# Kernel optimization log

Measured on AMD Instinct MI355X. Metric: run time of the kernel, lower is better.

The kernel has to match this reference:

```python
import jax, jax.numpy as jnp
import numpy as np

B, T, D, H, OUT = 256, 512, 512, 1024, 8


def setup_inputs() -> dict:
    key = jax.random.key(0)
    ks = jax.random.split(key, 7)
    s_ih = 1.0 / np.sqrt(H)
    return {
        "x": jax.random.normal(ks[0], (B, T, D), dtype=jnp.float32),
        "W_ih": jax.random.uniform(ks[1], (4 * H, D), minval=-s_ih, maxval=s_ih, dtype=jnp.float32),
        "W_hh": jax.random.uniform(ks[2], (4 * H, H), minval=-s_ih, maxval=s_ih, dtype=jnp.float32),
        "b_ih": jax.random.uniform(ks[3], (4 * H,), minval=-s_ih, maxval=s_ih, dtype=jnp.float32),
        "b_hh": jax.random.uniform(ks[4], (4 * H,), minval=-s_ih, maxval=s_ih, dtype=jnp.float32),
        "W_fc": jax.random.uniform(ks[5], (OUT, H), minval=-s_ih, maxval=s_ih, dtype=jnp.float32),
        "b_fc": jax.random.uniform(ks[6], (OUT,), minval=-s_ih, maxval=s_ih, dtype=jnp.float32),
    }


def reference(x, W_ih, W_hh, b_ih, b_hh, W_fc, b_fc):
    Bsz, Tlen, _ = x.shape
    Hd = W_hh.shape[1]
    # Precompute input-side gate projections for all time steps: [T, B, 4H]
    x_proj = jnp.einsum('btd,gd->tbg', x, W_ih) + b_ih + b_hh

    def step(carry, xp):
        h, c = carry
        gates = xp + h @ W_hh.T                 # [B, 4H]
        i, f, g, o = jnp.split(gates, 4, axis=-1)  # torch LSTMCell gate order
        i = jax.nn.sigmoid(i)
        f = jax.nn.sigmoid(f)
        g = jnp.tanh(g)
        o = jax.nn.sigmoid(o)
        c = f * c + i * g
        h = o * jnp.tanh(c)
        return (h, c), None

    h0 = jnp.zeros((Bsz, Hd), dtype=x.dtype)
    c0 = jnp.zeros((Bsz, Hd), dtype=x.dtype)
    (h, _), _ = jax.lax.scan(step, (h0, c0), x_proj)
    out = h @ W_fc.T + b_fc
    return jax.nn.sigmoid(out)
```

## Files before the change

kernel.cpp:

```cpp
#include <hip/hip_runtime.h>
#include <hip/hip_bf16.h>

#define Bsz 256
#define Tlen 512
#define Dd 512
#define Hh 1024
#define G4 4096
#define NOUT 8
#define BT (Bsz * Tlen)

typedef short s16x8 __attribute__((ext_vector_type(8)));
typedef unsigned short u16x8 __attribute__((ext_vector_type(8)));
typedef float f32x4 __attribute__((ext_vector_type(4)));

__device__ __forceinline__ ushort f2bf(float f) {
    union { float f; uint u; } v; v.f = f;
    uint u = v.u;
    uint r = u + 0x7FFFu + ((u >> 16) & 1u);
    return (ushort)(r >> 16);
}
__device__ __forceinline__ float bf2f(ushort u) {
    union { uint u; float f; } v; v.u = ((uint)u) << 16; return v.f;
}
__device__ __forceinline__ float sigf(float x) { return 1.f / (1.f + __expf(-x)); }
__device__ __forceinline__ float tanhfast(float x) {
    float ax = fabsf(x);
    float e = __expf(-2.f * ax);
    float t = (1.f - e) / (1.f + e);
    return copysignf(t, x);
}
__device__ __forceinline__ void gload16(const void* g, void* l) {
    __builtin_amdgcn_global_load_lds(
        (const __attribute__((address_space(1))) uint*)g,
        (__attribute__((address_space(3))) uint*)l, 16, 0, 0);
}

__global__ void init_kernel(uint4* __restrict__ h0, uint4* __restrict__ c) {
    int i = blockIdx.x * 256 + threadIdx.x;
    uint4 z = make_uint4(0u, 0u, 0u, 0u);
    c[i] = z;
    if (i < 32768) h0[i] = z;
}

__global__ void cvt_kernel(const float4* __restrict__ src, ushort4* __restrict__ dst, int n4) {
    int i = blockIdx.x * 256 + threadIdx.x;
    if (i >= n4) return;
    float4 v = src[i];
    ushort4 o;
    o.x = f2bf(v.x); o.y = f2bf(v.y); o.z = f2bf(v.z); o.w = f2bf(v.w);
    dst[i] = o;
}

__global__ void cvt_xchunk(const float* __restrict__ x, ushort* __restrict__ dst, int t0) {
    int gid = blockIdx.x * 256 + threadIdx.x;
    int k8  = gid & 63;
    int tl  = (gid >> 6) & 7;
    int row = gid >> 9;
    const float* s = x + ((size_t)row * Tlen + t0 + tl) * Dd + k8 * 8;
    float4 v0 = *(const float4*)s;
    float4 v1 = *(const float4*)(s + 4);
    u16x8 o;
    o[0]=f2bf(v0.x); o[1]=f2bf(v0.y); o[2]=f2bf(v0.z); o[3]=f2bf(v0.w);
    o[4]=f2bf(v1.x); o[5]=f2bf(v1.y); o[6]=f2bf(v1.z); o[7]=f2bf(v1.w);
    *(u16x8*)(dst + ((size_t)row * 8 + tl) * Dd + k8 * 8) = o;
}

__launch_bounds__(512, 2)
__global__ void lstm_step3(const ushort* __restrict__ xsrc, int tstride, int tloc,
                           const ushort* __restrict__ Wih,
                           const ushort* __restrict__ Whh,
                           const ushort* __restrict__ h_prev,
                           ushort* __restrict__ h_next,
                           float* __restrict__ c,
                           const float* __restrict__ b_ih,
                           const float* __restrict__ b_hh) {
    __shared__ char smem[131072];
    __shared__ float bias_lds[64];

    const int tid  = threadIdx.x;
    const int lane = tid & 63;
    const int w    = tid >> 6;
    const int g    = w >> 1;
    const int ab   = w & 1;

    const int B   = blockIdx.x;
    const int xcd  = B & 7, slot = B >> 3;
    const int jt   = xcd * 8 + (slot >> 2);
    const int bt   = slot & 3;
    const int b0   = bt * 64;

    if (tid < 64) {
        int gcol = (tid >> 4) * 1024 + jt * 16 + (tid & 15);
        bias_lds[tid] = b_ih[gcol] + b_hh[gcol];
    }

    f32x4 acc[4][2] = {};

    auto STAGE = [&](int buf, int it) {
        const int k0 = (g * 6 + it) << 6;
        char* base = smem + g * 32768 + buf * 16384 + ab * 8192;
        if (ab == 0) {
            if (k0 < Dd) {
                #pragma unroll
                for (int q = 0; q < 8; ++q) {
                    int r  = q * 8 + (lane >> 3);
                    int cs = (lane & 7) ^ (r & 7);
                    const ushort* gp = xsrc + ((size_t)(b0 + r) * tstride + tloc) * Dd + k0 + cs * 8;
                    gload16(gp, base + q * 1024);
                }
            } else {
                #pragma unroll
                for (int q = 0; q < 8; ++q) {
                    int r  = q * 8 + (lane >> 3);
                    int cs = (lane & 7) ^ (r & 7);
                    const ushort* gp = h_prev + (size_t)(b0 + r) * Hh + (k0 - Dd) + cs * 8;
                    gload16(gp, base + q * 1024);
                }
            }
        } else {
            #pragma unroll
            for (int q = 0; q < 8; ++q) {
                int col = q * 8 + (lane >> 3);
                int cs  = (lane & 7) ^ (col & 7);
                int grow = (col >> 4) * 1024 + jt * 16 + (col & 15);
                const ushort* gp = (k0 < Dd)
                    ? (Wih + (size_t)grow * Dd + k0 + cs * 8)
                    : (Whh + (size_t)grow * Hh + (k0 - Dd) + cs * 8);
                gload16(gp, base + q * 1024);
            }
        }
    };
    auto COMPUTE = [&](int buf) {
        const char* Ab = smem + g * 32768 + buf * 16384;
        const char* Bb = Ab + 8192;
        #pragma unroll
        for (int ks = 0; ks < 2; ++ks) {
            const int kc = (ks << 2) + (lane >> 4);
            s16x8 a[4], bb[2];
            #pragma unroll
            for (int m = 0; m < 4; ++m) {
                int row = (m << 4) + (lane & 15);
                a[m] = *(const s16x8*)(Ab + row * 128 + ((kc ^ (row & 7)) << 4));
            }
            #pragma unroll
            for (int n = 0; n < 2; ++n) {
                int col = (ab << 5) + (n << 4) + (lane & 15);
                bb[n] = *(const s16x8*)(Bb + col * 128 + ((kc ^ (col & 7)) << 4));
            }
            #pragma unroll
            for (int m = 0; m < 4; ++m)
                #pragma unroll
                for (int n = 0; n < 2; ++n)
                    acc[m][n] = __builtin_amdgcn_mfma_f32_16x16x32_bf16(a[m], bb[n], acc[m][n], 0, 0, 0);
        }
    };

    STAGE(0, 0);
    __syncthreads();
    #pragma unroll
    for (int it = 0; it < 6; ++it) {
        if (it < 5) STAGE((it + 1) & 1, it + 1);
        COMPUTE(it & 1);
        __syncthreads();
    }

    float* bw = (float*)smem + g * (64 * 68);
    #pragma unroll
    for (int m = 0; m < 4; ++m)
        #pragma unroll
        for (int n = 0; n < 2; ++n)
            #pragma unroll
            for (int j = 0; j < 4; ++j) {
                int row = (m << 4) + ((lane >> 4) << 2) + j;
                int col = (ab << 5) + (n << 4) + (lane & 15);
                bw[row * 68 + col] = acc[m][n][j];
            }
    __syncthreads();

    const float* bufs = (const float*)smem;
    #pragma unroll
    for (int u = 0; u < 2; ++u) {
        int cell = tid * 2 + u;
        int row  = cell >> 4;
        int cv   = cell & 15;
        float gi = 0.f, gf = 0.f, gg = 0.f, go = 0.f;
        #pragma unroll
        for (int p = 0; p < 4; ++p) {
            const float* bb = bufs + p * (64 * 68) + row * 68;
            gi += bb[cv]; gf += bb[16 + cv]; gg += bb[32 + cv]; go += bb[48 + cv];
        }
        gi += bias_lds[cv];      gf += bias_lds[16 + cv];
        gg += bias_lds[32 + cv]; go += bias_lds[48 + cv];
        float i_ = sigf(gi), f_ = sigf(gf), g_ = tanhfast(gg), o_ = sigf(go);
        int gcol = jt * 16 + cv;
        size_t cidx = (size_t)(b0 + row) * Hh + gcol;
        float cn = f_ * c[cidx] + i_ * g_;
        c[cidx] = cn;
        h_next[cidx] = f2bf(o_ * tanhfast(cn));
    }
}

__launch_bounds__(256)
__global__ void lstm_step_fused(const float* __restrict__ x,
                          const ushort* __restrict__ Wih,
                          const ushort* __restrict__ Whh,
                          const float* __restrict__ b_ih,
                          const float* __restrict__ b_hh,
                          const ushort* __restrict__ h_prev,
                          ushort* __restrict__ h_next,
                          float* __restrict__ c,
                          int t) {
    __shared__ ushort At[64 * 64];
    __shared__ ushort Bt[64 * 64];
    __shared__ float gates[64 * 72];

    const int tid  = threadIdx.x;
    const int lane = tid & 63;
    const int wid  = tid >> 6;
    const int wr   = wid >> 1;
    const int wc   = wid & 1;
    const int bt   = blockIdx.x >> 6;
    const int jt   = blockIdx.x & 63;
    const int b0   = bt * 64;
    const int j0   = jt * 16;

    f32x4 acc[2][2] = {};

    auto mfma_tile = [&]() {
        #pragma unroll
        for (int ks = 0; ks < 2; ++ks) {
            const int kc = (ks << 2) + (lane >> 4);
            s16x8 a[2], bfr[2];
            #pragma unroll
            for (int m = 0; m < 2; ++m) {
                int row = wr * 32 + m * 16 + (lane & 15);
                a[m] = *(const s16x8*)&At[row * 64 + ((kc ^ (row & 7)) << 3)];
            }
            #pragma unroll
            for (int n = 0; n < 2; ++n) {
                int col = wc * 32 + n * 16 + (lane & 15);
                bfr[n] = *(const s16x8*)&Bt[col * 64 + ((kc ^ (col & 7)) << 3)];
            }
            #pragma unroll
            for (int m = 0; m < 2; ++m)
                #pragma unroll
                for (int n = 0; n < 2; ++n)
                    acc[m][n] = __builtin_amdgcn_mfma_f32_16x16x32_bf16(a[m], bfr[n], acc[m][n], 0, 0, 0);
        }
    };

    for (int kb = 0; kb < Dd; kb += 64) {
        __syncthreads();
        #pragma unroll
        for (int it = 0; it < 4; ++it) {
            int idx = tid + it * 256;
            int row = idx >> 4;
            int k   = (idx & 15) * 4;
            const float4 v = *(const float4*)&x[(size_t)(b0 + row) * (Tlen * Dd) + (size_t)t * Dd + kb + k];
            ushort4 o;
            o.x = f2bf(v.x); o.y = f2bf(v.y); o.z = f2bf(v.z); o.w = f2bf(v.w);
            int dst = row * 64 + (((k >> 3) ^ (row & 7)) << 3) + (k & 7);
            *(ushort4*)&At[dst] = o;
        }
        #pragma unroll
        for (int it = 0; it < 2; ++it) {
            int idx = tid + it * 256;
            int col = idx >> 3;
            int kc  = idx & 7;
            int grow = ((col >> 4) << 10) + j0 + (col & 15);
            uint4 v = *(const uint4*)&Wih[(size_t)grow * Dd + kb + kc * 8];
            *(uint4*)&Bt[col * 64 + ((kc ^ (col & 7)) << 3)] = v;
        }
        __syncthreads();
        mfma_tile();
    }
    for (int kb = 0; kb < Hh; kb += 64) {
        __syncthreads();
        #pragma unroll
        for (int it = 0; it < 2; ++it) {
            int idx = tid + it * 256;
            int row = idx >> 3;
            int kc  = idx & 7;
            uint4 v = *(const uint4*)&h_prev[(size_t)(b0 + row) * Hh + kb + kc * 8];
            *(uint4*)&At[row * 64 + ((kc ^ (row & 7)) << 3)] = v;
        }
        #pragma unroll
        for (int it = 0; it < 2; ++it) {
            int idx = tid + it * 256;
            int col = idx >> 3;
            int kc  = idx & 7;
            int grow = ((col >> 4) << 10) + j0 + (col & 15);
            uint4 v = *(const uint4*)&Whh[(size_t)grow * Hh + kb + kc * 8];
            *(uint4*)&Bt[col * 64 + ((kc ^ (col & 7)) << 3)] = v;
        }
        __syncthreads();
        mfma_tile();
    }

    #pragma unroll
    for (int m = 0; m < 2; ++m)
        #pragma unroll
        for (int n = 0; n < 2; ++n)
            #pragma unroll
            for (int j = 0; j < 4; ++j) {
                int row = wr * 32 + m * 16 + ((lane >> 4) << 2) + j;
                int col = wc * 32 + n * 16 + (lane & 15);
                gates[row * 72 + col] = acc[m][n][j];
            }
    __syncthreads();

    #pragma unroll
    for (int it = 0; it < 4; ++it) {
        int idx = tid + it * 256;
        int row = idx >> 4;
        int cc  = idx & 15;
        int gcol = j0 + cc;
        float gi = gates[row * 72 + cc]      + b_ih[gcol]          + b_hh[gcol];
        float gf = gates[row * 72 + 16 + cc] + b_ih[Hh + gcol]     + b_hh[Hh + gcol];
        float gg = gates[row * 72 + 32 + cc] + b_ih[2 * Hh + gcol] + b_hh[2 * Hh + gcol];
        float go = gates[row * 72 + 48 + cc] + b_ih[3 * Hh + gcol] + b_hh[3 * Hh + gcol];
        float i_ = sigf(gi);
        float f_ = sigf(gf);
        float g_ = tanhfast(gg);
        float o_ = sigf(go);
        size_t cidx = (size_t)(b0 + row) * Hh + gcol;
        float cn = f_ * c[cidx] + i_ * g_;
        c[cidx] = cn;
        float hn = o_ * tanhfast(cn);
        h_next[cidx] = f2bf(hn);
    }
}

__global__ void fc_kernel(const ushort* __restrict__ h,
                          const float* __restrict__ Wfc,
                          const float* __restrict__ bfc,
                          float* __restrict__ out) {
    int b = blockIdx.x;
    int w = threadIdx.x >> 6;
    int lane = threadIdx.x & 63;
    float s = 0.f;
    for (int k = lane; k < Hh; k += 64)
        s += bf2f(h[(size_t)b * Hh + k]) * Wfc[w * Hh + k];
    #pragma unroll
    for (int off = 32; off; off >>= 1) s += __shfl_down(s, off);
    if (lane == 0) out[b * NOUT + w] = sigf(s + bfc[w]);
}


extern "C" void kernel_launch(void* const* d_in, const int* in_sizes, int n_in,
                              void* d_out, int out_size, void* d_ws, size_t ws_size,
                              hipStream_t stream) {
    const float* x    = (const float*)d_in[0];
    const float* W_ih = (const float*)d_in[1];
    const float* W_hh = (const float*)d_in[2];
    const float* b_ih = (const float*)d_in[3];
    const float* b_hh = (const float*)d_in[4];
    const float* W_fc = (const float*)d_in[5];
    const float* b_fc = (const float*)d_in[6];
    float* out = (float*)d_out;
    char* ws = (char*)d_ws;

    ushort* h_buf  = (ushort*)ws;
    float*  c_ws   = (float*)(ws + (1ull << 20));
    ushort* wih_bf = (ushort*)(ws + (2ull << 20));
    ushort* whh_bf = (ushort*)(ws + (6ull << 20));
    char*   x_ext  = ws + (14ull << 20);

    const size_t FIXED   = 14ull << 20;
    const size_t XFULL   = (size_t)Bsz * Tlen * Dd * 2;
    const size_t XCHUNK  = (size_t)Bsz * 8 * Dd * 2;

    init_kernel<<<256, 256, 0, stream>>>((uint4*)h_buf, (uint4*)c_ws);
    cvt_kernel<<<(G4 * Dd / 4) / 256, 256, 0, stream>>>((const float4*)W_ih, (ushort4*)wih_bf, G4 * Dd / 4);
    cvt_kernel<<<(G4 * Hh / 4) / 256, 256, 0, stream>>>((const float4*)W_hh, (ushort4*)whh_bf, G4 * Hh / 4);

    if (ws_size >= FIXED + XFULL) {
        ushort* x_bf = (ushort*)x_ext;
        const int n4 = BT * Dd / 4;
        cvt_kernel<<<n4 / 256, 256, 0, stream>>>((const float4*)x, (ushort4*)x_bf, n4);
        for (int t = 0; t < Tlen; ++t) {
            const ushort* hp = h_buf + (size_t)(t & 1) * Bsz * Hh;
            ushort*       hn = h_buf + (size_t)((t + 1) & 1) * Bsz * Hh;
            lstm_step3<<<256, 512, 0, stream>>>(x_bf, Tlen, t, wih_bf, whh_bf,
                                                hp, hn, c_ws, b_ih, b_hh);
        }
    } else if (ws_size >= FIXED + 2 * XCHUNK) {
        ushort* xchunk = (ushort*)x_ext;
        for (int t = 0; t < Tlen; ++t) {
            if ((t & 7) == 0) {
                ushort* dst = xchunk + (size_t)((t >> 3) & 1) * (Bsz * 8 * Dd);
                cvt_xchunk<<<512, 256, 0, stream>>>(x, dst, t);
            }
            const ushort* xb = xchunk + (size_t)((t >> 3) & 1) * (Bsz * 8 * Dd);
            const ushort* hp = h_buf + (size_t)(t & 1) * Bsz * Hh;
            ushort*       hn = h_buf + (size_t)((t + 1) & 1) * Bsz * Hh;
            lstm_step3<<<256, 512, 0, stream>>>(xb, 8, t & 7, wih_bf, whh_bf,
                                                hp, hn, c_ws, b_ih, b_hh);
        }
    } else {
        for (int t = 0; t < Tlen; ++t) {
            const ushort* hp = h_buf + (size_t)(t & 1) * Bsz * Hh;
            ushort*       hn = h_buf + (size_t)((t + 1) & 1) * Bsz * Hh;
            lstm_step_fused<<<256, 256, 0, stream>>>(x, wih_bf, whh_bf, b_ih, b_hh, hp, hn, c_ws, t);
        }
    }
    fc_kernel<<<256, 512, 0, stream>>>(h_buf, W_fc, b_fc, out);
}
```

Baseline: 5.618 ms.

## Load LSTM step operands directly into registers and split K across all eight waves

The per-step kernel no longer stages x/h and weight tiles through LDS with global_load_lds double buffering. Each of the 8 waves now owns 3 of the 24 K-chunks and loads A and B fragments straight from global memory into registers, with a two-deep software prefetch ahead of the MFMAs. Each wave computes the full 64x64 output tile, and the partial sums are reduced across 8 LDS buffers instead of 4. The aim is to drop LDS staging traffic and barriers inside the K loop. In exchange it uses more registers, issues uncoalesced 16-byte global loads without LDS reuse, and doubles the reduction work.

```diff
diff --git a/kernel.cpp b/kernel.cpp
--- a/kernel.cpp
+++ b/kernel.cpp
@@ -28,11 +28,6 @@
     float e = __expf(-2.f * ax);
     float t = (1.f - e) / (1.f + e);
     return copysignf(t, x);
-}
-__device__ __forceinline__ void gload16(const void* g, void* l) {
-    __builtin_amdgcn_global_load_lds(
-        (const __attribute__((address_space(1))) uint*)g,
-        (__attribute__((address_space(3))) uint*)l, 16, 0, 0);
 }
 
 __global__ void init_kernel(uint4* __restrict__ h0, uint4* __restrict__ c) {
@@ -66,7 +61,7 @@
 }
 
 __launch_bounds__(512, 2)
-__global__ void lstm_step3(const ushort* __restrict__ xsrc, int tstride, int tloc,
+__global__ void lstm_step4(const ushort* __restrict__ xsrc, int tstride, int tloc,
                            const ushort* __restrict__ Wih,
                            const ushort* __restrict__ Whh,
                            const ushort* __restrict__ h_prev,
@@ -74,16 +69,13 @@
                            float* __restrict__ c,
                            const float* __restrict__ b_ih,
                            const float* __restrict__ b_hh) {
-    __shared__ char smem[131072];
+    __shared__ float part[8][64 * 68];
     __shared__ float bias_lds[64];
 
     const int tid  = threadIdx.x;
     const int lane = tid & 63;
     const int w    = tid >> 6;
-    const int g    = w >> 1;
-    const int ab   = w & 1;
-
-    const int B   = blockIdx.x;
+    const int B    = blockIdx.x;
     const int xcd  = B & 7, slot = B >> 3;
     const int jt   = xcd * 8 + (slot >> 2);
     const int bt   = slot & 3;
@@ -94,106 +86,88 @@
         bias_lds[tid] = b_ih[gcol] + b_hh[gcol];
     }
 
-    f32x4 acc[4][2] = {};
-
-    auto STAGE = [&](int buf, int it) {
-        const int k0 = (g * 6 + it) << 6;
-        char* base = smem + g * 32768 + buf * 16384 + ab * 8192;
-        if (ab == 0) {
-            if (k0 < Dd) {
-                #pragma unroll
-                for (int q = 0; q < 8; ++q) {
-                    int r  = q * 8 + (lane >> 3);
-                    int cs = (lane & 7) ^ (r & 7);
-                    const ushort* gp = xsrc + ((size_t)(b0 + r) * tstride + tloc) * Dd + k0 + cs * 8;
-                    gload16(gp, base + q * 1024);
-                }
-            } else {
-                #pragma unroll
-                for (int q = 0; q < 8; ++q) {
-                    int r  = q * 8 + (lane >> 3);
-                    int cs = (lane & 7) ^ (r & 7);
-                    const ushort* gp = h_prev + (size_t)(b0 + r) * Hh + (k0 - Dd) + cs * 8;
-                    gload16(gp, base + q * 1024);
-                }
-            }
-        } else {
-            #pragma unroll
-            for (int q = 0; q < 8; ++q) {
-                int col = q * 8 + (lane >> 3);
-                int cs  = (lane & 7) ^ (col & 7);
-                int grow = (col >> 4) * 1024 + jt * 16 + (col & 15);
-                const ushort* gp = (k0 < Dd)
-                    ? (Wih + (size_t)grow * Dd + k0 + cs * 8)
-                    : (Whh + (size_t)grow * Hh + (k0 - Dd) + cs * 8);
-                gload16(gp, base + q * 1024);
+    const int rlo = lane & 15;
+    const int k8  = (lane >> 4) << 3;
+
+    auto loadA = [&](s16x8 (&a)[4][2], int cidx) {
+        const int kc = cidx << 6;
+        #pragma unroll
+        for (int ks = 0; ks < 2; ++ks) {
+            const int k = kc + (ks << 5) + k8;
+            #pragma unroll
+            for (int m = 0; m < 4; ++m) {
+                const int row = b0 + (m << 4) + rlo;
+                const ushort* p = (k < Dd)
+                    ? xsrc + ((size_t)row * tstride + tloc) * Dd + k
+                    : h_prev + (size_t)row * Hh + (k - Dd);
+                a[m][ks] = *(const s16x8*)p;
             }
         }
     };
-    auto COMPUTE = [&](int buf) {
-        const char* Ab = smem + g * 32768 + buf * 16384;
-        const char* Bb = Ab + 8192;
+    auto loadB = [&](s16x8 (&b)[4][2], int cidx) {
+        const int kc = cidx << 6;
         #pragma unroll
         for (int ks = 0; ks < 2; ++ks) {
-            const int kc = (ks << 2) + (lane >> 4);
-            s16x8 a[4], bb[2];
-            #pragma unroll
-            for (int m = 0; m < 4; ++m) {
-                int row = (m << 4) + (lane & 15);
-                a[m] = *(const s16x8*)(Ab + row * 128 + ((kc ^ (row & 7)) << 4));
-            }
-            #pragma unroll
-            for (int n = 0; n < 2; ++n) {
-                int col = (ab << 5) + (n << 4) + (lane & 15);
-                bb[n] = *(const s16x8*)(Bb + col * 128 + ((kc ^ (col & 7)) << 4));
-            }
+            const int k = kc + (ks << 5) + k8;
+            #pragma unroll
+            for (int n = 0; n < 4; ++n) {
+                const int grow = (n << 10) + (jt << 4) + rlo;
+                const ushort* p = (k < Dd)
+                    ? Wih + (size_t)grow * Dd + k
+                    : Whh + (size_t)grow * Hh + (k - Dd);
+                b[n][ks] = *(const s16x8*)p;
+            }
+        }
+    };
+
+    f32x4 acc[4][4] = {};
+    auto MFMA = [&](s16x8 (&a)[4][2], s16x8 (&b)[4][2]) {
+        #pragma unroll
+        for (int ks = 0; ks < 2; ++ks)
             #pragma unroll
             for (int m = 0; m < 4; ++m)
                 #pragma unroll
-                for (int n = 0; n < 2; ++n)
-                    acc[m][n] = __builtin_amdgcn_mfma_f32_16x16x32_bf16(a[m], bb[n], acc[m][n], 0, 0, 0);
-        }
+                for (int n = 0; n < 4; ++n)
+                    acc[m][n] = __builtin_amdgcn_mfma_f32_16x16x32_bf16(a[m][ks], b[n][ks], acc[m][n], 0, 0, 0);
     };
 
-    STAGE(0, 0);
-    __syncthreads();
-    #pragma unroll
-    for (int it = 0; it < 6; ++it) {
-        if (it < 5) STAGE((it + 1) & 1, it + 1);
-        COMPUTE(it & 1);
-        __syncthreads();
-    }
-
-    float* bw = (float*)smem + g * (64 * 68);
+    const int ch0 = w * 3;
+    s16x8 aA[4][2], bA[4][2], aB[4][2], bB[4][2];
+    loadA(aA, ch0);     loadB(bA, ch0);
+    loadA(aB, ch0 + 1); loadB(bB, ch0 + 1);
+    MFMA(aA, bA);
+    loadA(aA, ch0 + 2); loadB(bA, ch0 + 2);
+    MFMA(aB, bB);
+    MFMA(aA, bA);
+
+    float* bw = part[w];
     #pragma unroll
     for (int m = 0; m < 4; ++m)
         #pragma unroll
-        for (int n = 0; n < 2; ++n)
+        for (int n = 0; n < 4; ++n)
             #pragma unroll
             for (int j = 0; j < 4; ++j) {
                 int row = (m << 4) + ((lane >> 4) << 2) + j;
-                int col = (ab << 5) + (n << 4) + (lane & 15);
+                int col = (n << 4) + rlo;
                 bw[row * 68 + col] = acc[m][n][j];
             }
     __syncthreads();
 
-    const float* bufs = (const float*)smem;
+    const int cv = tid & 15;
+    const int r0 = (tid >> 4) << 1;
     #pragma unroll
     for (int u = 0; u < 2; ++u) {
-        int cell = tid * 2 + u;
-        int row  = cell >> 4;
-        int cv   = cell & 15;
-        float gi = 0.f, gf = 0.f, gg = 0.f, go = 0.f;
-        #pragma unroll
-        for (int p = 0; p < 4; ++p) {
-            const float* bb = bufs + p * (64 * 68) + row * 68;
+        const int row = r0 + u;
+        float gi = bias_lds[cv],      gf = bias_lds[16 + cv];
+        float gg = bias_lds[32 + cv], go = bias_lds[48 + cv];
+        #pragma unroll
+        for (int p = 0; p < 8; ++p) {
+            const float* bb = part[p] + row * 68;
             gi += bb[cv]; gf += bb[16 + cv]; gg += bb[32 + cv]; go += bb[48 + cv];
         }
-        gi += bias_lds[cv];      gf += bias_lds[16 + cv];
-        gg += bias_lds[32 + cv]; go += bias_lds[48 + cv];
         float i_ = sigf(gi), f_ = sigf(gf), g_ = tanhfast(gg), o_ = sigf(go);
-        int gcol = jt * 16 + cv;
-        size_t cidx = (size_t)(b0 + row) * Hh + gcol;
+        const int gcol = (jt << 4) + cv;
+        const size_t cidx = (size_t)(b0 + row) * Hh + gcol;
         float cn = f_ * c[cidx] + i_ * g_;
         c[cidx] = cn;
         h_next[cidx] = f2bf(o_ * tanhfast(cn));
@@ -381,7 +355,7 @@
         for (int t = 0; t < Tlen; ++t) {
             const ushort* hp = h_buf + (size_t)(t & 1) * Bsz * Hh;
             ushort*       hn = h_buf + (size_t)((t + 1) & 1) * Bsz * Hh;
-            lstm_step3<<<256, 512, 0, stream>>>(x_bf, Tlen, t, wih_bf, whh_bf,
+            lstm_step4<<<256, 512, 0, stream>>>(x_bf, Tlen, t, wih_bf, whh_bf,
                                                 hp, hn, c_ws, b_ih, b_hh);
         }
     } else if (ws_size >= FIXED + 2 * XCHUNK) {
@@ -394,7 +368,7 @@
             const ushort* xb = xchunk + (size_t)((t >> 3) & 1) * (Bsz * 8 * Dd);
             const ushort* hp = h_buf + (size_t)(t & 1) * Bsz * Hh;
             ushort*       hn = h_buf + (size_t)((t + 1) & 1) * Bsz * Hh;
-            lstm_step3<<<256, 512, 0, stream>>>(xb, 8, t & 7, wih_bf, whh_bf,
+            lstm_step4<<<256, 512, 0, stream>>>(xb, 8, t & 7, wih_bf, whh_bf,
                                                 hp, hn, c_ws, b_ih, b_hh);
         }
     } else {
```

After: 7.812 ms. 39.0% more time.

## Replace per-timestep launches with a persistent cooperative LSTM kernel using flag barriers

Applied to the files above, without the earlier changes.

Replaces 512 per-timestep kernel launches with one cooperative persistent kernel. Each block keeps its cell state in LDS, converts x to bf16 on the fly, and synchronises with dependent blocks through per-block flags in global memory using sc0/sc1 coherent loads and stores. This is meant to remove launch overhead and the separate x conversion pass. In exchange it relies on all 256 blocks being co-resident and on correct flag ordering, and the spin-wait can add its own latency.

```diff
diff --git a/kernel.cpp b/kernel.cpp
--- a/kernel.cpp
+++ b/kernel.cpp
@@ -12,6 +12,7 @@
 typedef short s16x8 __attribute__((ext_vector_type(8)));
 typedef unsigned short u16x8 __attribute__((ext_vector_type(8)));
 typedef float f32x4 __attribute__((ext_vector_type(4)));
+typedef uint u32x4 __attribute__((ext_vector_type(4)));
 
 __device__ __forceinline__ ushort f2bf(float f) {
     union { float f; uint u; } v; v.f = f;
@@ -33,6 +34,26 @@
     __builtin_amdgcn_global_load_lds(
         (const __attribute__((address_space(1))) uint*)g,
         (__attribute__((address_space(3))) uint*)l, 16, 0, 0);
+}
+__device__ __forceinline__ u32x4 scload16(const void* p) {
+    u32x4 r;
+    asm volatile("global_load_dwordx4 %0, %1, off sc0 sc1" : "=&v"(r) : "v"(p));
+    return r;
+}
+__device__ __forceinline__ int scload_u32(const int* p) {
+    int r;
+    asm volatile("global_load_dword %0, %1, off sc0 sc1\n\ts_waitcnt vmcnt(0)"
+                 : "=&v"(r) : "v"(p) : "memory");
+    return r;
+}
+__device__ __forceinline__ void scstore_u32(uint* p, uint v) {
+    asm volatile("global_store_dword %0, %1, off sc0 sc1" :: "v"(p), "v"(v) : "memory");
+}
+__device__ __forceinline__ u16x8 pack8(const float4& a, const float4& b) {
+    u16x8 o;
+    o[0]=f2bf(a.x); o[1]=f2bf(a.y); o[2]=f2bf(a.z); o[3]=f2bf(a.w);
+    o[4]=f2bf(b.x); o[5]=f2bf(b.y); o[6]=f2bf(b.z); o[7]=f2bf(b.w);
+    return o;
 }
 
 __global__ void init_kernel(uint4* __restrict__ h0, uint4* __restrict__ c) {
@@ -59,10 +80,197 @@
     const float* s = x + ((size_t)row * Tlen + t0 + tl) * Dd + k8 * 8;
     float4 v0 = *(const float4*)s;
     float4 v1 = *(const float4*)(s + 4);
-    u16x8 o;
-    o[0]=f2bf(v0.x); o[1]=f2bf(v0.y); o[2]=f2bf(v0.z); o[3]=f2bf(v0.w);
-    o[4]=f2bf(v1.x); o[5]=f2bf(v1.y); o[6]=f2bf(v1.z); o[7]=f2bf(v1.w);
-    *(u16x8*)(dst + ((size_t)row * 8 + tl) * Dd + k8 * 8) = o;
+    *(u16x8*)(dst + ((size_t)row * 8 + tl) * Dd + k8 * 8) = pack8(v0, v1);
+}
+
+__launch_bounds__(512, 1)
+__global__ void lstm_persist(const float* __restrict__ x,
+                             const ushort* __restrict__ Wih,
+                             const ushort* __restrict__ Whh,
+                             const float* __restrict__ b_ih,
+                             const float* __restrict__ b_hh,
+                             ushort* __restrict__ hbuf,
+                             int* __restrict__ flags) {
+    __shared__ char smem[131072];
+    __shared__ float c_lds[1024];
+    __shared__ float bias_lds[64];
+
+    const int tid  = threadIdx.x;
+    const int lane = tid & 63;
+    const int w    = tid >> 6;
+    const int g    = w >> 1;
+    const int ab   = w & 1;
+    const int B    = blockIdx.x;
+    const int xcd  = B & 7, slot = B >> 3;
+    const int jt   = xcd * 8 + (slot >> 2);
+    const int bt   = slot & 3;
+    const int b0   = bt * 64;
+    const int bidl = (lane >> 3) + ((lane & 7) << 5) + (bt << 3);
+
+    for (int i = tid; i < 1024; i += 512) c_lds[i] = 0.f;
+    if (tid < 64) {
+        int gcol = (tid >> 4) * 1024 + jt * 16 + (tid & 15);
+        bias_lds[tid] = b_ih[gcol] + b_hh[gcol];
+    }
+    __syncthreads();
+
+    char* Abase0 = smem + g * 32768;
+    float4 xv[16];
+    u32x4  hv[8];
+
+    #pragma unroll 1
+    for (int t = 1; t <= Tlen; ++t) {
+        const ushort* hrd = hbuf + (size_t)((t - 1) & 1) * (Bsz * Hh);
+        ushort*       hwr = hbuf + (size_t)(t & 1) * (Bsz * Hh);
+
+        f32x4 acc[4][2] = {};
+
+        auto ISSUE = [&](int it) {
+            const int k0 = g * 384 + it * 64;
+            if (ab == 0) {
+                if (k0 < Dd) {
+                    #pragma unroll
+                    for (int q = 0; q < 8; ++q) {
+                        int row = q * 8 + (lane >> 3);
+                        int cs  = (lane & 7) ^ (row & 7);
+                        const float* p = x + ((size_t)(b0 + row) * Tlen + (t - 1)) * Dd + k0 + cs * 8;
+                        xv[2*q]   = *(const float4*)p;
+                        xv[2*q+1] = *(const float4*)(p + 4);
+                    }
+                } else {
+                    #pragma unroll
+                    for (int q = 0; q < 8; ++q) {
+                        int row = q * 8 + (lane >> 3);
+                        int cs  = (lane & 7) ^ (row & 7);
+                        const ushort* p = hrd + (size_t)(b0 + row) * Hh + (k0 - Dd) + cs * 8;
+                        hv[q] = scload16(p);
+                    }
+                }
+            } else {
+                char* Bb = Abase0 + (it & 1) * 16384 + 8192;
+                #pragma unroll
+                for (int q = 0; q < 8; ++q) {
+                    int col = q * 8 + (lane >> 3);
+                    int cs  = (lane & 7) ^ (col & 7);
+                    int grow = ((col >> 4) << 10) + (jt << 4) + (col & 15);
+                    const ushort* p = (k0 < Dd)
+                        ? Wih + (size_t)grow * Dd + k0 + cs * 8
+                        : Whh + (size_t)grow * Hh + (k0 - Dd) + cs * 8;
+                    gload16(p, Bb + q * 1024);
+                }
+            }
+        };
+        auto WRITE = [&](int it) {
+            if (ab != 0) return;
+            const int k0 = g * 384 + it * 64;
+            char* Ab = Abase0 + (it & 1) * 16384;
+            if (k0 < Dd) {
+                #pragma unroll
+                for (int q = 0; q < 8; ++q)
+                    *(u16x8*)(Ab + q * 1024 + lane * 16) = pack8(xv[2*q], xv[2*q+1]);
+            } else {
+                asm volatile("s_waitcnt vmcnt(0)" ::: "memory");
+                __builtin_amdgcn_sched_barrier(0);
+                #pragma unroll
+                for (int q = 0; q < 8; ++q)
+                    *(u32x4*)(Ab + q * 1024 + lane * 16) = hv[q];
+            }
+        };
+        auto COMPUTE = [&](int buf) {
+            const char* Ab = Abase0 + buf * 16384;
+            const char* Bb = Ab + 8192;
+            #pragma unroll
+            for (int ks = 0; ks < 2; ++ks) {
+                const int kc = (ks << 2) + (lane >> 4);
+                s16x8 a[4], bb2[2];
+                #pragma unroll
+                for (int m = 0; m < 4; ++m) {
+                    int row = (m << 4) + (lane & 15);
+                    a[m] = *(const s16x8*)(Ab + row * 128 + ((kc ^ (row & 7)) << 4));
+                }
+                #pragma unroll
+                for (int n = 0; n < 2; ++n) {
+                    int col = (ab << 5) + (n << 4) + (lane & 15);
+                    bb2[n] = *(const s16x8*)(Bb + col * 128 + ((kc ^ (col & 7)) << 4));
+                }
+                #pragma unroll
+                for (int m = 0; m < 4; ++m)
+                    #pragma unroll
+                    for (int n = 0; n < 2; ++n)
+                        acc[m][n] = __builtin_amdgcn_mfma_f32_16x16x32_bf16(a[m], bb2[n], acc[m][n], 0, 0, 0);
+            }
+        };
+
+        ISSUE(0);
+        WRITE(0);
+        __syncthreads();
+        #pragma unroll
+        for (int it = 0; it < 6; ++it) {
+            if (it < 5) ISSUE(it + 1);
+            COMPUTE(it & 1);
+            if (it < 5) WRITE(it + 1);
+            __syncthreads();
+        }
+
+        float* bw = (float*)smem + g * (64 * 68);
+        #pragma unroll
+        for (int m = 0; m < 4; ++m)
+            #pragma unroll
+            for (int n = 0; n < 2; ++n)
+                #pragma unroll
+                for (int j = 0; j < 4; ++j) {
+                    int row = (m << 4) + ((lane >> 4) << 2) + j;
+                    int col = (ab << 5) + (n << 4) + (lane & 15);
+                    bw[row * 68 + col] = acc[m][n][j];
+                }
+        __syncthreads();
+
+        {
+            const float* part = (const float*)smem;
+            const int cell0 = tid * 2;
+            const int row = cell0 >> 4;
+            const int cv  = cell0 & 15;
+            float gv[2][4];
+            #pragma unroll
+            for (int u = 0; u < 2; ++u) {
+                gv[u][0] = bias_lds[cv + u];
+                gv[u][1] = bias_lds[16 + cv + u];
+                gv[u][2] = bias_lds[32 + cv + u];
+                gv[u][3] = bias_lds[48 + cv + u];
+            }
+            #pragma unroll
+            for (int p = 0; p < 4; ++p) {
+                const float* bb = part + p * (64 * 68) + row * 68;
+                #pragma unroll
+                for (int u = 0; u < 2; ++u) {
+                    gv[u][0] += bb[cv + u];
+                    gv[u][1] += bb[16 + cv + u];
+                    gv[u][2] += bb[32 + cv + u];
+                    gv[u][3] += bb[48 + cv + u];
+                }
+            }
+            ushort hn[2];
+            #pragma unroll
+            for (int u = 0; u < 2; ++u) {
+                float i_ = sigf(gv[u][0]), f_ = sigf(gv[u][1]);
+                float g_ = tanhfast(gv[u][2]), o_ = sigf(gv[u][3]);
+                float cn = f_ * c_lds[row * 16 + cv + u] + i_ * g_;
+                c_lds[row * 16 + cv + u] = cn;
+                hn[u] = f2bf(o_ * tanhfast(cn));
+            }
+            uint pack = (uint)hn[0] | ((uint)hn[1] << 16);
+            scstore_u32((uint*)(hwr + (size_t)(b0 + row) * Hh + (jt << 4) + cv), pack);
+        }
+
+        asm volatile("s_waitcnt vmcnt(0)" ::: "memory");
+        __syncthreads();
+        if (tid == 0) scstore_u32((uint*)&flags[B], (uint)t);
+        for (;;) {
+            int v = scload_u32(&flags[bidl]);
+            if (__all(v >= t)) break;
+            __builtin_amdgcn_s_sleep(4);
+        }
+    }
 }
 
 __launch_bounds__(512, 2)
@@ -362,17 +570,29 @@
 
     ushort* h_buf  = (ushort*)ws;
     float*  c_ws   = (float*)(ws + (1ull << 20));
+    int*    flags  = (int*)(ws + (1ull << 20));
     ushort* wih_bf = (ushort*)(ws + (2ull << 20));
     ushort* whh_bf = (ushort*)(ws + (6ull << 20));
     char*   x_ext  = ws + (14ull << 20);
 
-    const size_t FIXED   = 14ull << 20;
-    const size_t XFULL   = (size_t)Bsz * Tlen * Dd * 2;
-    const size_t XCHUNK  = (size_t)Bsz * 8 * Dd * 2;
+    const size_t FIXED  = 14ull << 20;
+    const size_t XFULL  = (size_t)Bsz * Tlen * Dd * 2;
+    const size_t XCHUNK = (size_t)Bsz * 8 * Dd * 2;
 
     init_kernel<<<256, 256, 0, stream>>>((uint4*)h_buf, (uint4*)c_ws);
     cvt_kernel<<<(G4 * Dd / 4) / 256, 256, 0, stream>>>((const float4*)W_ih, (ushort4*)wih_bf, G4 * Dd / 4);
     cvt_kernel<<<(G4 * Hh / 4) / 256, 256, 0, stream>>>((const float4*)W_hh, (ushort4*)whh_bf, G4 * Hh / 4);
+
+    {
+        void* args[] = { (void*)&x, (void*)&wih_bf, (void*)&whh_bf, (void*)&b_ih,
+                         (void*)&b_hh, (void*)&h_buf, (void*)&flags };
+        hipError_t err = hipLaunchCooperativeKernel((const void*)lstm_persist,
+                                                    dim3(256), dim3(512), args, 0, stream);
+        if (err == hipSuccess) {
+            fc_kernel<<<256, 512, 0, stream>>>(h_buf, W_fc, b_fc, out);
+            return;
+        }
+    }
 
     if (ws_size >= FIXED + XFULL) {
         ushort* x_bf = (ushort*)x_ext;
```

Result: slower. 11.29 ms (+100.9%).

## Hoist input projection into chunked GEMM, shrink per-step kernel to recurrent matmul

Applied to the files above, without the earlier changes.

Moves the x·W_ih projection out of the per-timestep LSTM kernel into a batched MFMA GEMM run every 8 timesteps, which writes gate pre-activations (with both biases) to a double-buffered workspace in fp32 or bf16. The per-step kernel then only multiplies h by W_hh over K=1024 and adds the precomputed projections. This cuts the per-step K dimension and the latency on the serial critical path. In exchange it adds extra launches and more memory traffic to write and read the projection buffers.

```diff
diff --git a/kernel.cpp b/kernel.cpp
--- a/kernel.cpp
+++ b/kernel.cpp
@@ -34,6 +34,10 @@
         (const __attribute__((address_space(1))) uint*)g,
         (__attribute__((address_space(3))) uint*)l, 16, 0, 0);
 }
+__device__ __forceinline__ void xp_store(ushort* p, float v) { *p = f2bf(v); }
+__device__ __forceinline__ void xp_store(float* p, float v) { *p = v; }
+__device__ __forceinline__ float xp_load(const ushort* p) { return bf2f(*p); }
+__device__ __forceinline__ float xp_load(const float* p) { return *p; }
 
 __global__ void init_kernel(uint4* __restrict__ h0, uint4* __restrict__ c) {
     int i = blockIdx.x * 256 + threadIdx.x;
@@ -63,6 +67,222 @@
     o[0]=f2bf(v0.x); o[1]=f2bf(v0.y); o[2]=f2bf(v0.z); o[3]=f2bf(v0.w);
     o[4]=f2bf(v1.x); o[5]=f2bf(v1.y); o[6]=f2bf(v1.z); o[7]=f2bf(v1.w);
     *(u16x8*)(dst + ((size_t)row * 8 + tl) * Dd + k8 * 8) = o;
+}
+
+template <typename XT>
+__launch_bounds__(256)
+__global__ void xproj_chunk(const float* __restrict__ x,
+                            const ushort* __restrict__ Wih,
+                            const float* __restrict__ b_ih,
+                            const float* __restrict__ b_hh,
+                            XT* __restrict__ xp, int t0) {
+    __shared__ ushort As[2][128 * 64];
+    __shared__ ushort Bs[2][128 * 64];
+    const int tid  = threadIdx.x;
+    const int lane = tid & 63;
+    const int wid  = tid >> 6;
+    const int wr   = wid >> 1;
+    const int wc   = wid & 1;
+    const int mt   = blockIdx.x >> 5;
+    const int nt   = blockIdx.x & 31;
+    const int m0   = mt * 128;
+    const int n0   = nt * 128;
+
+    f32x4 acc[4][4] = {};
+
+    auto stageA = [&](int buf, int kb) {
+        const int k0 = kb << 6;
+        #pragma unroll
+        for (int it = 0; it < 8; ++it) {
+            int idx = tid + (it << 8);
+            int row = idx >> 4;
+            int k   = (idx & 15) << 2;
+            int grow = m0 + row;
+            const float4 v = *(const float4*)&x[((size_t)(grow >> 3) * Tlen + t0 + (grow & 7)) * Dd + k0 + k];
+            ushort4 o;
+            o.x = f2bf(v.x); o.y = f2bf(v.y); o.z = f2bf(v.z); o.w = f2bf(v.w);
+            int dst = (row << 6) + (((k >> 3) ^ (row & 7)) << 3) + (k & 7);
+            *(ushort4*)&As[buf][dst] = o;
+        }
+    };
+    auto stageB = [&](int buf, int kb) {
+        const int k0 = kb << 6;
+        #pragma unroll
+        for (int ii = 0; ii < 4; ++ii) {
+            const int inst = (wid << 2) + ii;
+            const int r0 = inst << 3;
+            const int r  = r0 + (lane >> 3);
+            const int sw = ((lane & 7) ^ (r & 7)) << 3;
+            gload16(&Wih[(size_t)(n0 + r) * Dd + k0 + sw], &Bs[buf][r0 * 64]);
+        }
+    };
+    auto compute = [&](int buf) {
+        #pragma unroll
+        for (int ks = 0; ks < 2; ++ks) {
+            const int kc = (ks << 2) + (lane >> 4);
+            s16x8 a[4], b[4];
+            #pragma unroll
+            for (int m = 0; m < 4; ++m) {
+                int row = (wr << 6) + (m << 4) + (lane & 15);
+                a[m] = *(const s16x8*)&As[buf][row * 64 + ((kc ^ (row & 7)) << 3)];
+            }
+            #pragma unroll
+            for (int n = 0; n < 4; ++n) {
+                int col = (wc << 6) + (n << 4) + (lane & 15);
+                b[n] = *(const s16x8*)&Bs[buf][col * 64 + ((kc ^ (col & 7)) << 3)];
+            }
+            #pragma unroll
+            for (int m = 0; m < 4; ++m)
+                #pragma unroll
+                for (int n = 0; n < 4; ++n)
+                    acc[m][n] = __builtin_amdgcn_mfma_f32_16x16x32_bf16(a[m], b[n], acc[m][n], 0, 0, 0);
+        }
+    };
+
+    stageB(0, 0); stageA(0, 0);
+    __syncthreads();
+    for (int kb = 0; kb < 8; ++kb) {
+        if (kb < 7) { stageB((kb + 1) & 1, kb + 1); stageA((kb + 1) & 1, kb + 1); }
+        compute(kb & 1);
+        __syncthreads();
+    }
+
+    float bias[4];
+    #pragma unroll
+    for (int n = 0; n < 4; ++n) {
+        int gcol = n0 + (wc << 6) + (n << 4) + (lane & 15);
+        bias[n] = b_ih[gcol] + b_hh[gcol];
+    }
+    #pragma unroll
+    for (int m = 0; m < 4; ++m)
+        #pragma unroll
+        for (int n = 0; n < 4; ++n)
+            #pragma unroll
+            for (int j = 0; j < 4; ++j) {
+                int grow = m0 + (wr << 6) + (m << 4) + ((lane >> 4) << 2) + j;
+                int gcol = n0 + (wc << 6) + (n << 4) + (lane & 15);
+                int b_ = grow >> 3, tl = grow & 7;
+                xp_store(&xp[((size_t)tl * Bsz + b_) * G4 + gcol], acc[m][n][j] + bias[n]);
+            }
+}
+
+template <typename XT>
+__launch_bounds__(512, 2)
+__global__ void lstm_step9(const XT* __restrict__ xp,
+                           int tl,
+                           const ushort* __restrict__ Whh,
+                           const ushort* __restrict__ h_prev,
+                           ushort* __restrict__ h_next,
+                           float* __restrict__ c) {
+    __shared__ char smem[131072];
+
+    const int tid  = threadIdx.x;
+    const int lane = tid & 63;
+    const int w    = tid >> 6;
+    const int g    = w >> 1;
+    const int ab   = w & 1;
+    const int B    = blockIdx.x;
+    const int xcd  = B & 7, slot = B >> 3;
+    const int jt   = xcd * 8 + (slot >> 2);
+    const int bt   = slot & 3;
+    const int b0   = bt * 64;
+
+    const int erow = tid >> 3;
+    const int ecv  = (tid * 2) & 15;
+    const size_t cbase = (size_t)(b0 + erow) * Hh + (jt << 4) + ecv;
+    const float c0 = c[cbase], c1 = c[cbase + 1];
+    const XT* xpr = xp + ((size_t)tl * Bsz + b0 + erow) * G4 + (jt << 4) + ecv;
+    float xg[4][2];
+    #pragma unroll
+    for (int gi = 0; gi < 4; ++gi) {
+        xg[gi][0] = xp_load(xpr + gi * Hh);
+        xg[gi][1] = xp_load(xpr + gi * Hh + 1);
+    }
+
+    f32x4 acc[4][2] = {};
+
+    auto STAGE = [&](int buf, int it) {
+        const int k0 = (g << 8) + (it << 6);
+        char* base = smem + g * 32768 + buf * 16384 + ab * 8192;
+        if (ab == 0) {
+            #pragma unroll
+            for (int q = 0; q < 8; ++q) {
+                int r  = q * 8 + (lane >> 3);
+                int cs = (lane & 7) ^ (r & 7);
+                gload16(h_prev + (size_t)(b0 + r) * Hh + k0 + cs * 8, base + q * 1024);
+            }
+        } else {
+            #pragma unroll
+            for (int q = 0; q < 8; ++q) {
+                int col = q * 8 + (lane >> 3);
+                int cs  = (lane & 7) ^ (col & 7);
+                int grow = ((col >> 4) << 10) + (jt << 4) + (col & 15);
+                gload16(Whh + (size_t)grow * Hh + k0 + cs * 8, base + q * 1024);
+            }
+        }
+    };
+    auto COMPUTE = [&](int buf) {
+        const char* Ab = smem + g * 32768 + buf * 16384;
+        const char* Bb = Ab + 8192;
+        #pragma unroll
+        for (int ks = 0; ks < 2; ++ks) {
+            const int kc = (ks << 2) + (lane >> 4);
+            s16x8 a[4], bb[2];
+            #pragma unroll
+            for (int m = 0; m < 4; ++m) {
+                int row = (m << 4) + (lane & 15);
+                a[m] = *(const s16x8*)(Ab + row * 128 + ((kc ^ (row & 7)) << 4));
+            }
+            #pragma unroll
+            for (int n = 0; n < 2; ++n) {
+                int col = (ab << 5) + (n << 4) + (lane & 15);
+                bb[n] = *(const s16x8*)(Bb + col * 128 + ((kc ^ (col & 7)) << 4));
+            }
+            #pragma unroll
+            for (int m = 0; m < 4; ++m)
+                #pragma unroll
+                for (int n = 0; n < 2; ++n)
+                    acc[m][n] = __builtin_amdgcn_mfma_f32_16x16x32_bf16(a[m], bb[n], acc[m][n], 0, 0, 0);
+        }
+    };
+
+    STAGE(0, 0);
+    __syncthreads();
+    #pragma unroll
+    for (int it = 0; it < 4; ++it) {
+        if (it < 3) STAGE((it + 1) & 1, it + 1);
+        COMPUTE(it & 1);
+        __syncthreads();
+    }
+
+    float* bw = (float*)smem + g * (64 * 68);
+    #pragma unroll
+    for (int m = 0; m < 4; ++m)
+        #pragma unroll
+        for (int n = 0; n < 2; ++n)
+            #pragma unroll
+            for (int j = 0; j < 4; ++j) {
+                int row = (m << 4) + ((lane >> 4) << 2) + j;
+                int col = (ab << 5) + (n << 4) + (lane & 15);
+                bw[row * 68 + col] = acc[m][n][j];
+            }
+    __syncthreads();
+
+    const float* bufs = (const float*)smem;
+    #pragma unroll
+    for (int u = 0; u < 2; ++u) {
+        const int cv = ecv + u;
+        float gi = xg[0][u], gf = xg[1][u], gg = xg[2][u], go = xg[3][u];
+        #pragma unroll
+        for (int p = 0; p < 4; ++p) {
+            const float* bb = bufs + p * (64 * 68) + erow * 68;
+            gi += bb[cv]; gf += bb[16 + cv]; gg += bb[32 + cv]; go += bb[48 + cv];
+        }
+        float i_ = sigf(gi), f_ = sigf(gf), g_ = tanhfast(gg), o_ = sigf(go);
+        float cn = f_ * (u ? c1 : c0) + i_ * g_;
+        c[cbase + u] = cn;
+        h_next[cbase + u] = f2bf(o_ * tanhfast(cn));
+    }
 }
 
 __launch_bounds__(512, 2)
@@ -367,6 +587,9 @@
     char*   x_ext  = ws + (14ull << 20);
 
     const size_t FIXED   = 14ull << 20;
+    const size_t XPCH    = (size_t)8 * Bsz * G4;
+    const size_t NEEDF32 = FIXED + 2 * XPCH * 4;
+    const size_t NEEDB16 = FIXED + 2 * XPCH * 2;
     const size_t XFULL   = (size_t)Bsz * Tlen * Dd * 2;
     const size_t XCHUNK  = (size_t)Bsz * 8 * Dd * 2;
 
@@ -374,15 +597,27 @@
     cvt_kernel<<<(G4 * Dd / 4) / 256, 256, 0, stream>>>((const float4*)W_ih, (ushort4*)wih_bf, G4 * Dd / 4);
     cvt_kernel<<<(G4 * Hh / 4) / 256, 256, 0, stream>>>((const float4*)W_hh, (ushort4*)whh_bf, G4 * Hh / 4);
 
-    if (ws_size >= FIXED + XFULL) {
-        ushort* x_bf = (ushort*)x_ext;
-        const int n4 = BT * Dd / 4;
-        cvt_kernel<<<n4 / 256, 256, 0, stream>>>((const float4*)x, (ushort4*)x_bf, n4);
+    if (ws_size >= NEEDF32) {
+        float* xpb0 = (float*)x_ext;
+        float* xpb1 = xpb0 + XPCH;
         for (int t = 0; t < Tlen; ++t) {
+            float* xpb = ((t >> 3) & 1) ? xpb1 : xpb0;
+            if ((t & 7) == 0)
+                xproj_chunk<float><<<512, 256, 0, stream>>>(x, wih_bf, b_ih, b_hh, xpb, t);
             const ushort* hp = h_buf + (size_t)(t & 1) * Bsz * Hh;
             ushort*       hn = h_buf + (size_t)((t + 1) & 1) * Bsz * Hh;
-            lstm_step3<<<256, 512, 0, stream>>>(x_bf, Tlen, t, wih_bf, whh_bf,
-                                                hp, hn, c_ws, b_ih, b_hh);
+            lstm_step9<float><<<256, 512, 0, stream>>>(xpb, t & 7, whh_bf, hp, hn, c_ws);
+        }
+    } else if (ws_size >= NEEDB16) {
+        ushort* xpb0 = (ushort*)x_ext;
+        ushort* xpb1 = xpb0 + XPCH;
+        for (int t = 0; t < Tlen; ++t) {
+            ushort* xpb = ((t >> 3) & 1) ? xpb1 : xpb0;
+            if ((t & 7) == 0)
+                xproj_chunk<ushort><<<512, 256, 0, stream>>>(x, wih_bf, b_ih, b_hh, xpb, t);
+            const ushort* hp = h_buf + (size_t)(t & 1) * Bsz * Hh;
+            ushort*       hn = h_buf + (size_t)((t + 1) & 1) * Bsz * Hh;
+            lstm_step9<ushort><<<256, 512, 0, stream>>>(xpb, t & 7, whh_bf, hp, hn, c_ws);
         }
     } else if (ws_size >= FIXED + 2 * XCHUNK) {
         ushort* xchunk = (ushort*)x_ext;
```

Measured after the change: 5.331 ms. -5.1%, faster.
